# Optimization experiments

Measured on AMD Instinct MI355X. Metric: run time of the kernel, lower is better.

## Reference

```python
import jax, jax.numpy as jnp
import numpy as np


def _chamfer_sqmin(a, b):
    # a: [bs, N, 3], b: [bs, M, 3] -> min squared distance per a-point: [bs, N]
    a2 = jnp.sum(a * a, axis=-1)                     # [bs, N]
    b2 = jnp.sum(b * b, axis=-1)                     # [bs, M]
    ab = jnp.einsum('bnd,bmd->bnm', a, b)            # [bs, N, M]
    d = a2[:, :, None] + b2[:, None, :] - 2.0 * ab   # [bs, N, M] squared distances
    d = jnp.maximum(d, 0.0)                          # numerical floor
    return jnp.min(d, axis=-1)                       # [bs, N]


def setup_inputs() -> dict:
    key = jax.random.key(0)
    k1, k2 = jax.random.split(key)
    points = jax.random.normal(k1, (32, 4096, 3), dtype=jnp.float32)
    gts = jax.random.normal(k2, (32, 4096, 3), dtype=jnp.float32)
    return {"points": points, "gts": gts}


def reference(points, gts):
    p2g = _chamfer_sqmin(points, gts)   # [bs, N]
    g2p = _chamfer_sqmin(gts, points)   # [bs, M]
    p2g = jnp.mean(jnp.sqrt(p2g), axis=1)  # [bs]
    g2p = jnp.mean(jnp.sqrt(g2p), axis=1)  # [bs]
    loss = p2g + g2p
    return (jnp.mean(loss), jnp.mean(p2g), jnp.mean(g2p))
```

## Files before the change

kernel.cpp:

```cpp
#include <hip/hip_runtime.h>

typedef short short8 __attribute__((ext_vector_type(8)));
typedef float f32x16 __attribute__((ext_vector_type(16)));

#define NPTS 4096
#define NB   32
#define S    2
#define NT   (NPTS / 32)
#define SCALE (1.0f / 131072.0f)

__device__ inline unsigned short bf16_rne(float v) {
    unsigned u = __float_as_uint(v);
    unsigned r = u + 0x7FFFu + ((u >> 16) & 1u);
    return (unsigned short)(r >> 16);
}
__device__ inline float bf16_to_f(unsigned short h) {
    return __uint_as_float(((unsigned)h) << 16);
}
__device__ inline void bf_split(float v, unsigned short& h, unsigned short& l) {
    h = bf16_rne(v);
    l = bf16_rne(v - bf16_to_f(h));
}

__global__ __launch_bounds__(256) void pack_kernel(
    const float* __restrict__ points, const float* __restrict__ gts,
    unsigned short* __restrict__ pk, float* __restrict__ outp)
{
    const int tid = blockIdx.x * 256 + threadIdx.x;
    if (tid < 3) outp[tid] = 0.0f;
    const int c   = tid >> 17;
    const int rem = tid & 131071;
    const float* src = (c ? gts : points) + (size_t)rem * 3;
    const float x = src[0], y = src[1], z = src[2];
    const float hb = x * x + y * y + z * z;
    unsigned short xh, xl, yh, yl, zh, zl, hh, hl;
    bf_split(x, xh, xl); bf_split(y, yh, yl);
    bf_split(z, zh, zl); bf_split(hb, hh, hl);
    const unsigned short ONE = 0x3F80;
    unsigned short r[16] = { xh, yh, zh, ONE, hh,
                             xl, yl, zl, 0,   hl,
                             xh, yh, zh, ONE, hh, 0 };
    int4* dst = (int4*)(pk + (size_t)tid * 16);
    int4 w0, w1;
    w0.x = r[0] | (r[1] << 16);  w0.y = r[2]  | (r[3]  << 16);
    w0.z = r[4] | (r[5] << 16);  w0.w = r[6]  | (r[7]  << 16);
    w1.x = r[8] | (r[9] << 16);  w1.y = r[10] | (r[11] << 16);
    w1.z = r[12]| (r[13]<< 16);  w1.w = r[14] | (r[15] << 16);
    dst[0] = w0; dst[1] = w1;
}

__global__ __launch_bounds__(256, 4) void chamfer_main(
    const float* __restrict__ points, const float* __restrict__ gts,
    const unsigned short* __restrict__ pk, float* __restrict__ mins)
{
    const int d      = blockIdx.x;
    const int group  = d & 63;
    const int member = d >> 6;
    const int dir = group >> 5;
    const int b   = group & 31;

    const float* Ab = (dir ? gts : points) + (size_t)b * NPTS * 3;
    const int w = threadIdx.x >> 6, l = threadIdx.x & 63;
    const int half = l >> 5, c = l & 31;

    short8 af[S];
    #pragma unroll
    for (int s = 0; s < S; ++s) {
        const int i = member * 256 + w * 64 + s * 32 + c;
        const float ax = Ab[i * 3 + 0], ay = Ab[i * 3 + 1], az = Ab[i * 3 + 2];
        const float ha = ax * ax + ay * ay + az * az;
        unsigned short xh, xl, yh, yl, zh, zl, hh, hl;
        bf_split(-2.f * ax, xh, xl);
        bf_split(-2.f * ay, yh, yl);
        bf_split(-2.f * az, zh, zl);
        bf_split(ha, hh, hl);
        const unsigned short ONE = 0x3F80;
        short8 f;
        if (half == 0) {
            f[0]=(short)xh; f[1]=(short)yh; f[2]=(short)zh; f[3]=(short)hh;
            f[4]=(short)ONE; f[5]=(short)xh; f[6]=(short)yh; f[7]=(short)zh;
        } else {
            f[0]=(short)hh; f[1]=(short)ONE; f[2]=(short)xl; f[3]=(short)yl;
            f[4]=(short)zl; f[5]=(short)hl; f[6]=0; f[7]=0;
        }
        af[s] = f;
    }

    const unsigned short* rec =
        pk + (((size_t)(dir ^ 1) * NB + b) * NPTS + (size_t)c) * 16 + half * 8;

    float mm[S] = {1e30f, 1e30f};

#define TREE3(A, MM)                                                           \
    {                                                                          \
        float t0, t1, t2, t3, t4, u0, u1;                                      \
        asm("v_min3_f32 %0, %1, %2, %3" : "=v"(t0)                             \
            : "v"((A)[0]),  "v"((A)[1]),  "v"((A)[2]));                        \
        asm("v_min3_f32 %0, %1, %2, %3" : "=v"(t1)                             \
            : "v"((A)[3]),  "v"((A)[4]),  "v"((A)[5]));                        \
        asm("v_min3_f32 %0, %1, %2, %3" : "=v"(t2)                             \
            : "v"((A)[6]),  "v"((A)[7]),  "v"((A)[8]));                        \
        asm("v_min3_f32 %0, %1, %2, %3" : "=v"(t3)                             \
            : "v"((A)[9]),  "v"((A)[10]), "v"((A)[11]));                       \
        asm("v_min3_f32 %0, %1, %2, %3" : "=v"(t4)                             \
            : "v"((A)[12]), "v"((A)[13]), "v"((A)[14]));                       \
        asm("v_min3_f32 %0, %1, %2, %3" : "=v"(u0)                             \
            : "v"(t0), "v"(t1), "v"(t2));                                      \
        asm("v_min3_f32 %0, %1, %2, %3" : "=v"(u1)                             \
            : "v"(t3), "v"(t4), "v"((A)[15]));                                 \
        asm("v_min3_f32 %0, %0, %1, %2" : "+v"(MM)                             \
            : "v"(u0), "v"(u1));                                               \
    }

#define UNIT(REG)                                                              \
    {                                                                          \
        f32x16 a0, a1;                                                         \
        asm volatile(                                                          \
            "v_mfma_f32_32x32x16_bf16 %0, %2, %3, 0\n\t"                       \
            "v_mfma_f32_32x32x16_bf16 %1, %2, %4, 0\n\t"                       \
            "s_nop 7\n\t"                                                      \
            "s_nop 7\n\t"                                                      \
            "s_nop 7\n\t"                                                      \
            "s_nop 7\n\t"                                                      \
            "s_nop 7"                                                          \
            : "=&v"(a0), "=&v"(a1)                                             \
            : "v"(REG), "v"(af[0]), "v"(af[1]));                               \
        TREE3(a0, mm[0])                                                       \
        TREE3(a1, mm[1])                                                       \
        __builtin_amdgcn_sched_barrier(0);                                     \
    }

#define LD(I) (*(const short8*)(rec + (size_t)((I) < NT ? (I) : NT - 1) * 512))

    short8 b0 = LD(0);
    short8 b1 = LD(1);
    short8 b2 = LD(2);

    #pragma unroll 1
    for (int t = 0; t < NT - 2; t += 3) {
        UNIT(b0) b0 = LD(t + 3);
        UNIT(b1) b1 = LD(t + 4);
        UNIT(b2) b2 = LD(t + 5);
    }
    UNIT(b0)
    UNIT(b1)
#undef LD
#undef UNIT
#undef TREE3

    #pragma unroll
    for (int s = 0; s < S; ++s) {
        float v = fminf(mm[s], __shfl_xor(mm[s], 32));
        v = fmaxf(v, 0.f);
        if (half == 0) {
            const int ap = member * 256 + w * 64 + s * 32 + c;
            mins[(size_t)group * NPTS + ap] = v;
        }
    }
}

__global__ __launch_bounds__(256) void reduce_kernel(
    const float* __restrict__ mins, float* __restrict__ outp)
{
    const int group = blockIdx.x;
    const int dir   = group >> 5;
    const float* gm = mins + (size_t)group * NPTS;

    float local = 0.f;
    #pragma unroll
    for (int i = 0; i < NPTS / 256; ++i)
        local += sqrtf(gm[threadIdx.x + i * 256]);

    for (int off = 32; off > 0; off >>= 1)
        local += __shfl_down(local, off);
    __shared__ float wsum[4];
    const int w = threadIdx.x >> 6, l = threadIdx.x & 63;
    if (l == 0) wsum[w] = local;
    __syncthreads();
    if (threadIdx.x == 0) {
        const float s = (wsum[0] + wsum[1] + wsum[2] + wsum[3]) * SCALE;
        atomicAdd(&outp[0], s);
        atomicAdd(&outp[1 + dir], s);
    }
}

extern "C" void kernel_launch(void* const* d_in, const int* in_sizes, int n_in,
                              void* d_out, int out_size, void* d_ws, size_t ws_size,
                              hipStream_t stream) {
    const float* points = (const float*)d_in[0];
    const float* gts    = (const float*)d_in[1];
    float* outp = (float*)d_out;

    unsigned short* packed = (unsigned short*)((char*)d_ws + 64);
    float* mins = (float*)((char*)d_ws + 64 + 8388608);

    pack_kernel<<<1024, 256, 0, stream>>>(points, gts, packed, outp);
    chamfer_main<<<1024, 256, 0, stream>>>(points, gts, packed, mins);
    reduce_kernel<<<64, 256, 0, stream>>>(mins, outp);
}
```

Baseline: 48.89 us.

## Tile four A-fragments per wave and split B range into chunks with atomicMin

Each wave now holds four A-point fragments instead of two, so every loaded B fragment feeds four MFMAs rather than two, which halves B-load traffic per MFMA. To keep the grid at 1024 blocks, the B point range is split into two chunks. Partial minima are merged with atomicMin on the float bit patterns, which works because the values are clamped non-negative, and the pack kernel initialises the mins buffer to FLT_MAX. This raises register pressure under launch_bounds(256,4) and adds global atomics plus an extra init write.

```diff
diff --git a/kernel.cpp b/kernel.cpp
--- a/kernel.cpp
+++ b/kernel.cpp
@@ -5,8 +5,10 @@
 
 #define NPTS 4096
 #define NB   32
-#define S    2
-#define NT   (NPTS / 32)
+#define S    4
+#define CHUNKS 2
+#define BPTS (NPTS / CHUNKS)
+#define NT   (BPTS / 32)
 #define SCALE (1.0f / 131072.0f)
 
 __device__ inline unsigned short bf16_rne(float v) {
@@ -24,7 +26,8 @@
 
 __global__ __launch_bounds__(256) void pack_kernel(
     const float* __restrict__ points, const float* __restrict__ gts,
-    unsigned short* __restrict__ pk, float* __restrict__ outp)
+    unsigned short* __restrict__ pk, unsigned* __restrict__ minsInit,
+    float* __restrict__ outp)
 {
     const int tid = blockIdx.x * 256 + threadIdx.x;
     if (tid < 3) outp[tid] = 0.0f;
@@ -47,15 +50,17 @@
     w1.x = r[8] | (r[9] << 16);  w1.y = r[10] | (r[11] << 16);
     w1.z = r[12]| (r[13]<< 16);  w1.w = r[14] | (r[15] << 16);
     dst[0] = w0; dst[1] = w1;
+    minsInit[tid] = 0x7F7FFFFFu;
 }
 
 __global__ __launch_bounds__(256, 4) void chamfer_main(
     const float* __restrict__ points, const float* __restrict__ gts,
-    const unsigned short* __restrict__ pk, float* __restrict__ mins)
+    const unsigned short* __restrict__ pk, unsigned* __restrict__ minsU)
 {
     const int d      = blockIdx.x;
     const int group  = d & 63;
-    const int member = d >> 6;
+    const int member = (d >> 6) & 7;
+    const int chunk  = d >> 9;
     const int dir = group >> 5;
     const int b   = group & 31;
 
@@ -66,7 +71,7 @@
     short8 af[S];
     #pragma unroll
     for (int s = 0; s < S; ++s) {
-        const int i = member * 256 + w * 64 + s * 32 + c;
+        const int i = member * 512 + w * 128 + s * 32 + c;
         const float ax = Ab[i * 3 + 0], ay = Ab[i * 3 + 1], az = Ab[i * 3 + 2];
         const float ha = ax * ax + ay * ay + az * az;
         unsigned short xh, xl, yh, yl, zh, zl, hh, hl;
@@ -87,9 +92,10 @@
     }
 
     const unsigned short* rec =
-        pk + (((size_t)(dir ^ 1) * NB + b) * NPTS + (size_t)c) * 16 + half * 8;
-
-    float mm[S] = {1e30f, 1e30f};
+        pk + (((size_t)(dir ^ 1) * NB + b) * NPTS + (size_t)chunk * BPTS + c) * 16
+           + half * 8;
+
+    float mm[S] = {1e30f, 1e30f, 1e30f, 1e30f};
 
 #define TREE3(A, MM)                                                           \
     {                                                                          \
@@ -114,19 +120,23 @@
 
 #define UNIT(REG)                                                              \
     {                                                                          \
-        f32x16 a0, a1;                                                         \
+        f32x16 a0, a1, a2, a3;                                                 \
         asm volatile(                                                          \
-            "v_mfma_f32_32x32x16_bf16 %0, %2, %3, 0\n\t"                       \
-            "v_mfma_f32_32x32x16_bf16 %1, %2, %4, 0\n\t"                       \
+            "v_mfma_f32_32x32x16_bf16 %0, %4, %5, 0\n\t"                       \
+            "v_mfma_f32_32x32x16_bf16 %1, %4, %6, 0\n\t"                       \
+            "v_mfma_f32_32x32x16_bf16 %2, %4, %7, 0\n\t"                       \
+            "v_mfma_f32_32x32x16_bf16 %3, %4, %8, 0\n\t"                       \
             "s_nop 7\n\t"                                                      \
             "s_nop 7\n\t"                                                      \
             "s_nop 7\n\t"                                                      \
             "s_nop 7\n\t"                                                      \
             "s_nop 7"                                                          \
-            : "=&v"(a0), "=&v"(a1)                                             \
-            : "v"(REG), "v"(af[0]), "v"(af[1]));                               \
+            : "=&v"(a0), "=&v"(a1), "=&v"(a2), "=&v"(a3)                       \
+            : "v"(REG), "v"(af[0]), "v"(af[1]), "v"(af[2]), "v"(af[3]));       \
         TREE3(a0, mm[0])                                                       \
         TREE3(a1, mm[1])                                                       \
+        TREE3(a2, mm[2])                                                       \
+        TREE3(a3, mm[3])                                                       \
         __builtin_amdgcn_sched_barrier(0);                                     \
     }
 
@@ -143,7 +153,6 @@
         UNIT(b2) b2 = LD(t + 5);
     }
     UNIT(b0)
-    UNIT(b1)
 #undef LD
 #undef UNIT
 #undef TREE3
@@ -153,8 +162,8 @@
         float v = fminf(mm[s], __shfl_xor(mm[s], 32));
         v = fmaxf(v, 0.f);
         if (half == 0) {
-            const int ap = member * 256 + w * 64 + s * 32 + c;
-            mins[(size_t)group * NPTS + ap] = v;
+            const int ap = member * 512 + w * 128 + s * 32 + c;
+            atomicMin(&minsU[(size_t)group * NPTS + ap], __float_as_uint(v));
         }
     }
 }
@@ -192,9 +201,9 @@
     float* outp = (float*)d_out;
 
     unsigned short* packed = (unsigned short*)((char*)d_ws + 64);
-    float* mins = (float*)((char*)d_ws + 64 + 8388608);
-
-    pack_kernel<<<1024, 256, 0, stream>>>(points, gts, packed, outp);
+    unsigned* mins = (unsigned*)((char*)d_ws + 64 + 8388608);
+
+    pack_kernel<<<1024, 256, 0, stream>>>(points, gts, packed, mins, outp);
     chamfer_main<<<1024, 256, 0, stream>>>(points, gts, packed, mins);
-    reduce_kernel<<<64, 256, 0, stream>>>(mins, outp);
-}
+    reduce_kernel<<<64, 256, 0, stream>>>((const float*)mins, outp);
+}
```

New measurement: 48.06 us. No clear change (-1.7%).
